# Kernel optimization log

Measured on AMD Instinct MI355X. Metric: run time of the kernel, lower is better.

## Reference

```python
import jax, jax.numpy as jnp
import numpy as np

N = 100000   # nodes
E = 1600000  # edges
D = 64       # in_channels
H = 64       # hidden_channels
G = 1000     # number of graphs (100 nodes each)


def _xavier(key, fan_in, fan_out):
    a = np.sqrt(6.0 / (fan_in + fan_out)).astype(np.float32)
    return jax.random.uniform(key, (fan_in, fan_out), jnp.float32, -a, a)


def setup_inputs() -> dict:
    key = jax.random.key(0)
    ks = jax.random.split(key, 6)
    x = jax.random.normal(ks[0], (N, D), jnp.float32)
    edge_index = jax.random.randint(ks[1], (2, E), 0, N, dtype=jnp.int32)
    edge_weight = jax.random.uniform(ks[2], (E,), jnp.float32)
    # every graph id 0..G-1 occurs exactly N//G times (sorted)
    batch = (jnp.arange(N, dtype=jnp.int32) // (N // G)).astype(jnp.int32)
    W1 = _xavier(ks[3], D, H); b1 = jnp.zeros((H,), jnp.float32)
    W2 = _xavier(ks[4], H, H); b2 = jnp.zeros((H,), jnp.float32)
    W3 = _xavier(ks[5], H, 1); b3 = jnp.zeros((1,), jnp.float32)
    return dict(x=x, edge_index=edge_index, edge_weight=edge_weight, batch=batch,
                W1=W1, b1=b1, W2=W2, b2=b2, W3=W3, b3=b3)


def reference(x, edge_index, edge_weight, batch, W1, b1, W2, b2, W3, b3):
    src, dst = edge_index[0], edge_index[1]
    # nodes per graph (torch.bincount(batch)) and broadcast back to nodes
    counts = jax.ops.segment_sum(jnp.ones((N,), jnp.float32), batch, num_segments=G)
    cpn = counts[batch]  # [N]

    def mpnn_layer(h, W, b):
        # gather x_j, scale by edge weight, scatter-add to target nodes
        m = h[src] * edge_weight[:, None]              # [E, C]
        agg = jax.ops.segment_sum(m, dst, num_segments=N)  # [N, C]
        out = agg / cpn[:, None]                       # per-node normalize
        return out @ W + b

    h = jax.nn.sigmoid(mpnn_layer(x, W1, b1))
    h = jax.nn.sigmoid(mpnn_layer(h, W2, b2))
    h = mpnn_layer(h, W3, b3)                          # [N, 1]
    # global mean pool over each graph
    pooled = jax.ops.segment_sum(h, batch, num_segments=G) / counts[:, None]
    return pooled  # [G, 1]
```

## Files before the change

kernel.cpp:

```cpp
#include <hip/hip_runtime.h>
#include <hip/hip_fp16.h>
#include <math.h>

#define NN 100000
#define EE 1600000
#define GG 1000
#define NPG 100
#define NBUK 391
#define BCAP 4608
#define EPB 8192
#define NBINBLK ((EE + EPB - 1) / EPB)
#define GEMM1BLK ((NN + 127) / 128)
#define GEMM2BLK ((NN + 63) / 64)

typedef __attribute__((ext_vector_type(8))) short short8v;
typedef __attribute__((ext_vector_type(4))) float float4v;

__device__ __forceinline__ unsigned char f32_to_fp8(float a) {
    return (unsigned char)(__builtin_amdgcn_cvt_pk_fp8_f32(a, a, 0, false) & 0xFF);
}
__device__ __forceinline__ float fp8_to_f32(unsigned b) {
    return __builtin_amdgcn_cvt_f32_fp8((int)b, 0);
}
__device__ __forceinline__ unsigned short f32_to_bf16(float f) {
    unsigned u = __float_as_uint(f);
    unsigned r = u + 0x7FFFu + ((u >> 16) & 1u);
    return (unsigned short)(r >> 16);
}

#if __has_builtin(__builtin_amdgcn_cvt_pk_f32_fp8)
typedef float floatx2 __attribute__((ext_vector_type(2)));
#define HAVE_PK_CVT 1
#else
#define HAVE_PK_CVT 0
#endif

__device__ __forceinline__ void unpack4(unsigned dw, float* f) {
#if HAVE_PK_CVT
    floatx2 lo = __builtin_amdgcn_cvt_pk_f32_fp8(dw, false);
    floatx2 hi = __builtin_amdgcn_cvt_pk_f32_fp8(dw, true);
    f[0] = lo.x; f[1] = lo.y; f[2] = hi.x; f[3] = hi.y;
#else
    f[0] = fp8_to_f32(dw & 0xFF);
    f[1] = fp8_to_f32((dw >> 8) & 0xFF);
    f[2] = fp8_to_f32((dw >> 16) & 0xFF);
    f[3] = fp8_to_f32((dw >> 24) & 0xFF);
#endif
}

__device__ __forceinline__ float4v mfma16(short8v a, short8v b, float4v c) {
    return __builtin_amdgcn_mfma_f32_16x16x32_bf16(a, b, c, 0, 0, 0);
}
__device__ __forceinline__ short8v fp8x8_to_bf16frag(uint2 q) {
    float f[8];
    unpack4(q.x, f);
    unpack4(q.y, f + 4);
    short8v s;
#pragma unroll
    for (int j = 0; j < 8; j++) s[j] = (short)f32_to_bf16(f[j]);
    return s;
}
__device__ __forceinline__ short8v f32x8_to_bf16frag(float4 a, float4 b) {
    short8v s;
    s[0] = (short)f32_to_bf16(a.x); s[1] = (short)f32_to_bf16(a.y);
    s[2] = (short)f32_to_bf16(a.z); s[3] = (short)f32_to_bf16(a.w);
    s[4] = (short)f32_to_bf16(b.x); s[5] = (short)f32_to_bf16(b.y);
    s[6] = (short)f32_to_bf16(b.z); s[7] = (short)f32_to_bf16(b.w);
    return s;
}
template<int NT>
__device__ __forceinline__ void stageW(const float* __restrict__ W,
                                       unsigned short* Wt, int tid) {
    for (int i = tid; i < 4096; i += NT) {
        int k = i >> 6, c = i & 63;
        Wt[(c << 6) | (((k >> 3) ^ (c & 7)) << 3) | (k & 7)] = f32_to_bf16(W[i]);
    }
}
__device__ __forceinline__ short8v ldB(const unsigned short* Wt, int col, int g) {
    return *(const short8v*)&Wt[(col << 6) | ((g ^ (col & 7)) << 3)];
}
__device__ __forceinline__ void mfma_tile_store(short8v a_lo, short8v a_hi,
                                                const unsigned short* Wt,
                                                int row0, int lane,
                                                unsigned char* __restrict__ out, int n) {
    int rl = lane & 15, kg = lane >> 4;
#pragma unroll
    for (int ct = 0; ct < 4; ct++) {
        int col = ct * 16 + rl;
        short8v blo = ldB(Wt, col, kg);
        short8v bhi = ldB(Wt, col, 4 + kg);
        float4v acc = {0.f, 0.f, 0.f, 0.f};
        acc = mfma16(a_lo, blo, acc);
        acc = mfma16(a_hi, bhi, acc);
        int dr = (lane >> 4) * 4;
#pragma unroll
        for (int r = 0; r < 4; r++) {
            int R = row0 + dr + r;
            if (R < n) out[(size_t)R * 64 + col] = f32_to_fp8(acc[r]);
        }
    }
}

__global__ __launch_bounds__(512)
void k_binbound(const int* __restrict__ src, const int* __restrict__ dst,
                const float* __restrict__ ew, int* __restrict__ bukcnt,
                uint2* __restrict__ ep1, int* __restrict__ rowptr, int E) {
    __shared__ int hist[NBUK];
    __shared__ int gbase[NBUK];
    int tid = threadIdx.x;
    if (blockIdx.x == 0 && tid == 0) rowptr[NN] = EE;
    for (int i = tid; i < NBUK; i += 512) hist[i] = 0;
    __syncthreads();
    int base = blockIdx.x * EPB;
    int b[16], rank[16];
    unsigned x[16], w[16];
#pragma unroll
    for (int u = 0; u < 16; u++) {
        int e = base + u * 512 + tid;
        if (e < E) {
            int d = dst[e];
            b[u] = d >> 8;
            x[u] = ((unsigned)(d & 255) << 24) | (unsigned)src[e];
            w[u] = __float_as_uint(ew[e]);
            rank[u] = atomicAdd(&hist[b[u]], 1);
        } else b[u] = -1;
    }
    __syncthreads();
    for (int i = tid; i < NBUK; i += 512) {
        int h = hist[i];
        gbase[i] = h ? atomicAdd(&bukcnt[i], h) : 0;
    }
    __syncthreads();
#pragma unroll
    for (int u = 0; u < 16; u++) {
        if (b[u] >= 0) ep1[(size_t)b[u] * BCAP + gbase[b[u]] + rank[u]] = make_uint2(x[u], w[u]);
    }
}

__global__ __launch_bounds__(512)
void k_bin2gemm1(const uint2* __restrict__ ep1, const int* __restrict__ bukcnt,
                 unsigned* __restrict__ ep2, int* __restrict__ rowptr,
                 const float* __restrict__ x, const float* __restrict__ W1,
                 unsigned char* __restrict__ t, int n) {
    __shared__ __align__(16) unsigned char smem[41984];
    int tid = threadIdx.x;
    int bk = blockIdx.x;
    if (bk < NBUK) {
        uint2* stage = (uint2*)smem;
        int* h   = (int*)(smem + 36864);
        int* s   = h + 256;
        int* cur = s + 256;
        int* sc  = cur + 256;
        int v = (tid < NBUK) ? bukcnt[tid] : 0;
        sc[tid] = v;
        __syncthreads();
        for (int off = 1; off < 512; off <<= 1) {
            int tv = (tid >= off) ? sc[tid - off] : 0;
            __syncthreads();
            sc[tid] += tv;
            __syncthreads();
        }
        int cnt = bukcnt[bk];
        int base = sc[bk] - cnt;
        if (tid < 256) h[tid] = 0;
        __syncthreads();
        size_t ebase = (size_t)bk * BCAP;
        for (int e = tid; e < cnt; e += 512) {
            uint2 r = ep1[ebase + e];
            stage[e] = r;
            atomicAdd(&h[r.x >> 24], 1);
        }
        __syncthreads();
        if (tid < 256) s[tid] = h[tid];
        __syncthreads();
        for (int off = 1; off < 256; off <<= 1) {
            int tv = 0;
            if (tid < 256 && tid >= off) tv = s[tid - off];
            __syncthreads();
            if (tid < 256) s[tid] += tv;
            __syncthreads();
        }
        if (tid < 256) {
            int pfx = base + s[tid] - h[tid];
            int node = bk * 256 + tid;
            if (node < n) rowptr[node] = pfx;
            cur[tid] = pfx;
        }
        __syncthreads();
        for (int e = tid; e < cnt; e += 512) {
            uint2 r = stage[e];
            int pos = atomicAdd(&cur[r.x >> 24], 1);
            unsigned wq = (unsigned)fminf(__uint_as_float(r.y) * 32768.f + 0.5f, 32767.f);
            ep2[pos] = (wq << 17) | (r.x & 0x1FFFFu);
        }
    } else {
        unsigned short* Wt = (unsigned short*)smem;
        stageW<512>(W1, Wt, tid);
        __syncthreads();
        int w = tid >> 6, lane = tid & 63;
        int row0 = (bk - NBUK) * 128 + w * 16;
        int rl = lane & 15, kg = lane >> 4;
        int rsrc = row0 + rl;
        if (rsrc > n - 1) rsrc = n - 1;
        const float* ar = x + (size_t)rsrc * 64 + kg * 8;
        float4 f0 = *(const float4*)ar;
        float4 f1 = *(const float4*)(ar + 4);
        float4 f2 = *(const float4*)(ar + 32);
        float4 f3 = *(const float4*)(ar + 36);
        short8v a_lo = f32x8_to_bf16frag(f0, f1);
        short8v a_hi = f32x8_to_bf16frag(f2, f3);
        mfma_tile_store(a_lo, a_hi, Wt, row0, lane, t, n);
    }
}

__global__ __launch_bounds__(256)
void k_gemm64_mfma(const unsigned char* __restrict__ inp, const float* __restrict__ W,
                   unsigned char* __restrict__ out, int n) {
    __shared__ __align__(16) unsigned short Wt[64 * 64];
    int tid = threadIdx.x;
    stageW<256>(W, Wt, tid);
    __syncthreads();
    int w = tid >> 6, lane = tid & 63;
    int row0 = blockIdx.x * 64 + w * 16;
    int rl = lane & 15, kg = lane >> 4;
    int rsrc = row0 + rl;
    if (rsrc > n - 1) rsrc = n - 1;
    const unsigned char* ar = inp + (size_t)rsrc * 64 + kg * 8;
    uint2 qlo = *(const uint2*)ar;
    uint2 qhi = *(const uint2*)(ar + 32);
    short8v a_lo = fp8x8_to_bf16frag(qlo);
    short8v a_hi = fp8x8_to_bf16frag(qhi);
    mfma_tile_store(a_lo, a_hi, Wt, row0, lane, out, n);
}

template<int MODE>
__global__ void k_gather64(const unsigned char* __restrict__ t, const int* __restrict__ rowptr,
                           const unsigned* __restrict__ ep, void* __restrict__ outp,
                           const float* __restrict__ bv, const float* __restrict__ W3,
                           int n) {
    int wid = (blockIdx.x * blockDim.x + threadIdx.x) >> 6;
    int lane = threadIdx.x & 63;
    wid = __builtin_amdgcn_readfirstlane(wid);
    if (wid >= n) return;
    int beg = rowptr[wid], end = rowptr[wid + 1];
    int deg = end - beg;
    float acc0 = 0.f, acc1 = 0.f;
    if (deg > 0) {
        int nfull = deg >> 4;
        int e = beg;
        unsigned r0[16], r1[16];
#pragma unroll
        for (int u = 0; u < 16; u++) r0[u] = ep[e + u];
        for (int b = 0; b < nfull; b++) {
#pragma unroll
            for (int u = 0; u < 16; u++) r1[u] = ep[e + 16 + u];
#pragma unroll
            for (int u = 0; u < 16; u++) {
                unsigned off = (r0[u] & 0x1FFFFu) * 64u + (unsigned)lane;
                float v = fp8_to_f32(t[off]);
                if (u & 1) acc1 = fmaf((float)(r0[u] >> 17), v, acc1);
                else       acc0 = fmaf((float)(r0[u] >> 17), v, acc0);
            }
#pragma unroll
            for (int u = 0; u < 16; u++) r0[u] = r1[u];
            e += 16;
        }
        int rem = deg & 15;
        if (rem) {
#pragma unroll
            for (int u = 0; u < 16; u++) {
                unsigned rm = (u < rem) ? r0[u] : 0u;
                unsigned off = (rm & 0x1FFFFu) * 64u + (unsigned)lane;
                float v = fp8_to_f32(t[off]);
                if (u & 1) acc1 = fmaf((float)(rm >> 17), v, acc1);
                else       acc0 = fmaf((float)(rm >> 17), v, acc0);
            }
        }
    }
    const float C = 0x1p-15f / (float)NPG;
    float v = (acc0 + acc1) * C + bv[lane];
    v = 1.f / (1.f + __expf(-v));
    if (MODE == 0) {
        ((unsigned char*)outp)[(size_t)wid * 64 + lane] = f32_to_fp8(v);
    } else {
        v *= W3[lane];
#pragma unroll
        for (int off = 32; off > 0; off >>= 1) v += __shfl_down(v, off, 64);
        if (lane == 0) ((float*)outp)[wid] = v;
    }
}

__global__ __launch_bounds__(256)
void k_y3pool(const float* __restrict__ y, const int* __restrict__ rowptr,
              const unsigned* __restrict__ ep,
              const float* __restrict__ b3, float* __restrict__ out) {
    __shared__ float red[256];
    int g = blockIdx.x;
    int tid = threadIdx.x;
    int ebeg = rowptr[g * NPG], eend = rowptr[g * NPG + NPG];
    float acc = 0.f;
    for (int e = ebeg + tid; e < eend; e += 256) {
        unsigned r = ep[e];
        unsigned off = (r & 0x1FFFFu) * 4u;
        acc = fmaf((float)(r >> 17), *(const float*)((const char*)y + off), acc);
    }
    red[tid] = acc;
    __syncthreads();
    for (int off = 128; off > 0; off >>= 1) {
        if (tid < off) red[tid] += red[tid + off];
        __syncthreads();
    }
    if (tid == 0) {
        out[g] = red[0] * 0x1p-15f / ((float)NPG * (float)NPG) + b3[0];
    }
}

extern "C" void kernel_launch(void* const* d_in, const int* in_sizes, int n_in,
                              void* d_out, int out_size, void* d_ws, size_t ws_size,
                              hipStream_t stream) {
    const float* x     = (const float*)d_in[0];
    const int*   ei    = (const int*)d_in[1];
    const int*   src   = ei;
    const int*   dst   = ei + EE;
    const float* ew    = (const float*)d_in[2];
    const float* W1    = (const float*)d_in[4];
    const float* b1    = (const float*)d_in[5];
    const float* W2    = (const float*)d_in[6];
    const float* b2    = (const float*)d_in[7];
    const float* W3    = (const float*)d_in[8];
    const float* b3    = (const float*)d_in[9];
    float* out = (float*)d_out;

    unsigned char* t   = (unsigned char*)d_ws;
    unsigned char* t2  = t + (size_t)NN * 64;
    unsigned char* hh8 = t2 + (size_t)NN * 64;
    float* y      = (float*)(hh8 + (size_t)NN * 64);
    unsigned* ep2 = (unsigned*)(y + NN);
    int*   bukcnt = (int*)(ep2 + EE);
    int*   rowptr = bukcnt + NBUK + 1;
    uint2* ep1    = (uint2*)(rowptr + NN + 2);

    hipMemsetAsync(bukcnt, 0, NBUK * sizeof(int), stream);

    k_binbound<<<NBINBLK, 512, 0, stream>>>(src, dst, ew, bukcnt, ep1, rowptr, EE);

    k_bin2gemm1<<<NBUK + GEMM1BLK, 512, 0, stream>>>(ep1, bukcnt, ep2, rowptr, x, W1, t, NN);

    int gblk = (int)(((size_t)NN * 64 + 255) / 256);

    k_gather64<0><<<gblk, 256, 0, stream>>>(t, rowptr, ep2, hh8, b1, nullptr, NN);

    k_gemm64_mfma<<<GEMM2BLK, 256, 0, stream>>>(hh8, W2, t2, NN);

    k_gather64<1><<<gblk, 256, 0, stream>>>(t2, rowptr, ep2, y, b2, W3, NN);

    k_y3pool<<<GG, 256, 0, stream>>>(y, rowptr, ep2, b3, out);
}
```

Baseline: 215.6 us.

## Process 16 nodes per wave in gather with software-pipelined edge chunks

The gather kernel now assigns 16 consecutive destination nodes to each wavefront and streams their CSR edges as one continuous run. Edge words and fp8 feature bytes are double-buffered: the next chunk's loads are issued before the current chunk's FMAs, and each node's epilogue fires when its edge boundary is crossed. This targets per-node launch and tail overhead (waves with few edges, remainder handling) and aims to hide gather latency, at the cost of more registers and a serial boundary check inside the inner loop. Occupancy is also pinned through launch bounds.

```diff
diff --git a/kernel.cpp b/kernel.cpp
--- a/kernel.cpp
+++ b/kernel.cpp
@@ -6,6 +6,7 @@
 #define EE 1600000
 #define GG 1000
 #define NPG 100
+#define NPW 16
 #define NBUK 391
 #define BCAP 4608
 #define EPB 8192
@@ -234,60 +235,92 @@
 }
 
 template<int MODE>
-__global__ void k_gather64(const unsigned char* __restrict__ t, const int* __restrict__ rowptr,
-                           const unsigned* __restrict__ ep, void* __restrict__ outp,
-                           const float* __restrict__ bv, const float* __restrict__ W3,
-                           int n) {
-    int wid = (blockIdx.x * blockDim.x + threadIdx.x) >> 6;
+__global__ __launch_bounds__(256, 4)
+void k_gather64(const unsigned char* __restrict__ t, const int* __restrict__ rowptr,
+                const unsigned* __restrict__ ep, void* __restrict__ outp,
+                const float* __restrict__ bv, const float* __restrict__ W3,
+                int nw) {
+    int gwid = (blockIdx.x * blockDim.x + threadIdx.x) >> 6;
     int lane = threadIdx.x & 63;
-    wid = __builtin_amdgcn_readfirstlane(wid);
-    if (wid >= n) return;
-    int beg = rowptr[wid], end = rowptr[wid + 1];
-    int deg = end - beg;
-    float acc0 = 0.f, acc1 = 0.f;
-    if (deg > 0) {
-        int nfull = deg >> 4;
-        int e = beg;
-        unsigned r0[16], r1[16];
-#pragma unroll
-        for (int u = 0; u < 16; u++) r0[u] = ep[e + u];
-        for (int b = 0; b < nfull; b++) {
-#pragma unroll
-            for (int u = 0; u < 16; u++) r1[u] = ep[e + 16 + u];
-#pragma unroll
-            for (int u = 0; u < 16; u++) {
-                unsigned off = (r0[u] & 0x1FFFFu) * 64u + (unsigned)lane;
-                float v = fp8_to_f32(t[off]);
-                if (u & 1) acc1 = fmaf((float)(r0[u] >> 17), v, acc1);
-                else       acc0 = fmaf((float)(r0[u] >> 17), v, acc0);
-            }
-#pragma unroll
-            for (int u = 0; u < 16; u++) r0[u] = r1[u];
-            e += 16;
-        }
-        int rem = deg & 15;
-        if (rem) {
-#pragma unroll
-            for (int u = 0; u < 16; u++) {
-                unsigned rm = (u < rem) ? r0[u] : 0u;
-                unsigned off = (rm & 0x1FFFFu) * 64u + (unsigned)lane;
-                float v = fp8_to_f32(t[off]);
-                if (u & 1) acc1 = fmaf((float)(rm >> 17), v, acc1);
-                else       acc0 = fmaf((float)(rm >> 17), v, acc0);
-            }
-        }
-    }
-    const float C = 0x1p-15f / (float)NPG;
-    float v = (acc0 + acc1) * C + bv[lane];
-    v = 1.f / (1.f + __expf(-v));
-    if (MODE == 0) {
-        ((unsigned char*)outp)[(size_t)wid * 64 + lane] = f32_to_fp8(v);
-    } else {
-        v *= W3[lane];
-#pragma unroll
-        for (int off = 32; off > 0; off >>= 1) v += __shfl_down(v, off, 64);
-        if (lane == 0) ((float*)outp)[wid] = v;
-    }
+    gwid = __builtin_amdgcn_readfirstlane(gwid);
+    if (gwid >= nw) return;
+    int n0 = gwid * NPW;
+    int n1 = n0 + NPW; if (n1 > NN) n1 = NN;
+    int li = lane < (n1 - n0) ? lane : (n1 - n0);
+    int rv = rowptr[n0 + li];
+    int eb   = __builtin_amdgcn_readfirstlane(__shfl(rv, 0, 64));
+    int eend = __builtin_amdgcn_readfirstlane(__shfl(rv, n1 - n0, 64));
+    int j = n0;
+    int end_j = __builtin_amdgcn_readlane(rv, 1);
+    int nch = (eend - eb + 15) >> 4;
+    float acc = 0.f;
+    const float Cn = 0x1p-15f / (float)NPG;
+    float bvl = bv[lane];
+    float w3l = (MODE == 1) ? W3[lane] : 0.f;
+
+    auto epi = [&]() {
+        float vv = acc * Cn + bvl;
+        vv = 1.f / (1.f + __expf(-vv));
+        if (MODE == 0) {
+            ((unsigned char*)outp)[(size_t)j * 64 + lane] = f32_to_fp8(vv);
+        } else {
+            vv *= w3l;
+            vv += __shfl_down(vv, 32, 64);
+            vv += __shfl_down(vv, 16, 64);
+            vv += __shfl_down(vv, 8, 64);
+            vv += __shfl_down(vv, 4, 64);
+            vv += __shfl_down(vv, 2, 64);
+            vv += __shfl_down(vv, 1, 64);
+            if (lane == 0) ((float*)outp)[j] = vv;
+        }
+        acc = 0.f;
+    };
+
+#define LOADW(W, cc) { _Pragma("unroll") \
+    for (int u = 0; u < 16; u++) W[u] = ep[eb + (cc) * 16 + u]; }
+
+#define ISSUEB(B, WT, W, cc) { _Pragma("unroll") \
+    for (int u = 0; u < 16; u++) { \
+        unsigned wd = (eb + (cc) * 16 + u < eend) ? W[u] : 0u; \
+        WT[u] = (float)(wd >> 17); \
+        B[u] = (unsigned)t[(wd & 0x1FFFFu) * 64u + (unsigned)lane]; \
+    } }
+
+#define FMACHUNK(B, WT, cc) { _Pragma("unroll") \
+    for (int u = 0; u < 16; u++) { \
+        int ee = eb + (cc) * 16 + u; \
+        while (j < n1 && ee == end_j) { \
+            epi(); \
+            j++; \
+            end_j = __builtin_amdgcn_readlane(rv, j - n0 + 1); \
+        } \
+        acc = fmaf(WT[u], fp8_to_f32(B[u]), acc); \
+    } }
+
+    if (nch > 0) {
+        unsigned wA[16], wB[16], b0[16], b1[16];
+        float wt0[16], wt1[16];
+        LOADW(wA, 0);
+        if (nch > 1) LOADW(wB, 1);
+        ISSUEB(b0, wt0, wA, 0);
+        int c = 0;
+        while (true) {
+            if (c + 1 < nch) ISSUEB(b1, wt1, wB, c + 1);
+            if (c + 2 < nch) LOADW(wA, c + 2);
+            FMACHUNK(b0, wt0, c);
+            c++;
+            if (c >= nch) break;
+            if (c + 1 < nch) ISSUEB(b0, wt0, wA, c + 1);
+            if (c + 2 < nch) LOADW(wB, c + 2);
+            FMACHUNK(b1, wt1, c);
+            c++;
+            if (c >= nch) break;
+        }
+    }
+    while (j < n1) { epi(); j++; }
+#undef LOADW
+#undef ISSUEB
+#undef FMACHUNK
 }
 
 __global__ __launch_bounds__(256)
@@ -346,13 +379,14 @@
 
     k_bin2gemm1<<<NBUK + GEMM1BLK, 512, 0, stream>>>(ep1, bukcnt, ep2, rowptr, x, W1, t, NN);
 
-    int gblk = (int)(((size_t)NN * 64 + 255) / 256);
-
-    k_gather64<0><<<gblk, 256, 0, stream>>>(t, rowptr, ep2, hh8, b1, nullptr, NN);
+    int nwv = (NN + NPW - 1) / NPW;
+    int gblk = (nwv * 64 + 255) / 256;
+
+    k_gather64<0><<<gblk, 256, 0, stream>>>(t, rowptr, ep2, hh8, b1, nullptr, nwv);
 
     k_gemm64_mfma<<<GEMM2BLK, 256, 0, stream>>>(hh8, W2, t2, NN);
 
-    k_gather64<1><<<gblk, 256, 0, stream>>>(t2, rowptr, ep2, y, b2, W3, NN);
+    k_gather64<1><<<gblk, 256, 0, stream>>>(t2, rowptr, ep2, y, b2, W3, nwv);
 
     k_y3pool<<<GG, 256, 0, stream>>>(y, rowptr, ep2, b3, out);
 }
```

After: 266.9 us. 1.24x slower.

## Gather 4 fp8 channels per lane across 4 edges with shuffled edge indices

Applied to the files above, without the earlier changes.

Restructures the per-node gather so each wavefront loads up to 64 edge records in one coalesced read and broadcasts them with shuffles. Each lane then reads a 4-byte chunk (4 fp8 channels), so four quarter-waves handle four edges at a time, and the partial sums are combined with xor shuffles. This replaces many byte-wide scalar loads and the per-edge serial loop with wider vector loads and more edges in flight, at the cost of cross-lane reductions and idle lanes for low-degree nodes. The output path packs 4 fp8 values per store, and the final W3 dot product is adjusted to match.

```diff
diff --git a/kernel.cpp b/kernel.cpp
--- a/kernel.cpp
+++ b/kernel.cpp
@@ -234,59 +234,72 @@
 }
 
 template<int MODE>
-__global__ void k_gather64(const unsigned char* __restrict__ t, const int* __restrict__ rowptr,
-                           const unsigned* __restrict__ ep, void* __restrict__ outp,
-                           const float* __restrict__ bv, const float* __restrict__ W3,
-                           int n) {
+__global__ __launch_bounds__(256)
+void k_gather64(const unsigned char* __restrict__ t, const int* __restrict__ rowptr,
+                const unsigned* __restrict__ ep, void* __restrict__ outp,
+                const float* __restrict__ bv, const float* __restrict__ W3,
+                int n) {
     int wid = (blockIdx.x * blockDim.x + threadIdx.x) >> 6;
     int lane = threadIdx.x & 63;
     wid = __builtin_amdgcn_readfirstlane(wid);
     if (wid >= n) return;
     int beg = rowptr[wid], end = rowptr[wid + 1];
-    int deg = end - beg;
-    float acc0 = 0.f, acc1 = 0.f;
-    if (deg > 0) {
-        int nfull = deg >> 4;
-        int e = beg;
-        unsigned r0[16], r1[16];
-#pragma unroll
-        for (int u = 0; u < 16; u++) r0[u] = ep[e + u];
-        for (int b = 0; b < nfull; b++) {
-#pragma unroll
-            for (int u = 0; u < 16; u++) r1[u] = ep[e + 16 + u];
-#pragma unroll
-            for (int u = 0; u < 16; u++) {
-                unsigned off = (r0[u] & 0x1FFFFu) * 64u + (unsigned)lane;
-                float v = fp8_to_f32(t[off]);
-                if (u & 1) acc1 = fmaf((float)(r0[u] >> 17), v, acc1);
-                else       acc0 = fmaf((float)(r0[u] >> 17), v, acc0);
+    int q = lane >> 4;
+    unsigned sl4 = (unsigned)(lane & 15) * 4u;
+    float ax = 0.f, ay = 0.f, az = 0.f, aw = 0.f;
+    for (int base = beg; base < end; base += 64) {
+        int el = base + lane;
+        unsigned wl = 0u;
+        if (el < end) wl = ep[el];
+        int nE = end - base; if (nE > 64) nE = 64;
+        int ng = (nE + 3) >> 2;
+        for (int g0 = 0; g0 < ng; g0 += 4) {
+            unsigned vv[4];
+            float wt[4];
+#pragma unroll
+            for (int p = 0; p < 4; p++) {
+                unsigned wq = __shfl(wl, (g0 + p) * 4 + q, 64);
+                wt[p] = (float)(wq >> 17);
+                vv[p] = *(const unsigned*)(t + ((wq & 0x1FFFFu) * 64u + sl4));
             }
 #pragma unroll
-            for (int u = 0; u < 16; u++) r0[u] = r1[u];
-            e += 16;
-        }
-        int rem = deg & 15;
-        if (rem) {
-#pragma unroll
-            for (int u = 0; u < 16; u++) {
-                unsigned rm = (u < rem) ? r0[u] : 0u;
-                unsigned off = (rm & 0x1FFFFu) * 64u + (unsigned)lane;
-                float v = fp8_to_f32(t[off]);
-                if (u & 1) acc1 = fmaf((float)(rm >> 17), v, acc1);
-                else       acc0 = fmaf((float)(rm >> 17), v, acc0);
+            for (int p = 0; p < 4; p++) {
+                float f[4];
+                unpack4(vv[p], f);
+                ax = fmaf(wt[p], f[0], ax);
+                ay = fmaf(wt[p], f[1], ay);
+                az = fmaf(wt[p], f[2], az);
+                aw = fmaf(wt[p], f[3], aw);
             }
         }
     }
-    const float C = 0x1p-15f / (float)NPG;
-    float v = (acc0 + acc1) * C + bv[lane];
-    v = 1.f / (1.f + __expf(-v));
+    ax += __shfl_xor(ax, 16, 64); ax += __shfl_xor(ax, 32, 64);
+    ay += __shfl_xor(ay, 16, 64); ay += __shfl_xor(ay, 32, 64);
+    az += __shfl_xor(az, 16, 64); az += __shfl_xor(az, 32, 64);
+    aw += __shfl_xor(aw, 16, 64); aw += __shfl_xor(aw, 32, 64);
+
+    const float Cn = 0x1p-15f / (float)NPG;
+    float4 bb = ((const float4*)bv)[lane & 15];
+    float v0 = ax * Cn + bb.x, v1 = ay * Cn + bb.y;
+    float v2 = az * Cn + bb.z, v3 = aw * Cn + bb.w;
+    v0 = 1.f / (1.f + __expf(-v0));
+    v1 = 1.f / (1.f + __expf(-v1));
+    v2 = 1.f / (1.f + __expf(-v2));
+    v3 = 1.f / (1.f + __expf(-v3));
     if (MODE == 0) {
-        ((unsigned char*)outp)[(size_t)wid * 64 + lane] = f32_to_fp8(v);
+        if (q == 0) {
+            unsigned r = (unsigned)__builtin_amdgcn_cvt_pk_fp8_f32(v0, v1, 0, false);
+            r = (unsigned)__builtin_amdgcn_cvt_pk_fp8_f32(v2, v3, (int)r, true);
+            ((unsigned*)outp)[(size_t)wid * 16 + (lane & 15)] = r;
+        }
     } else {
-        v *= W3[lane];
-#pragma unroll
-        for (int off = 32; off > 0; off >>= 1) v += __shfl_down(v, off, 64);
-        if (lane == 0) ((float*)outp)[wid] = v;
+        float4 w4 = ((const float4*)W3)[lane & 15];
+        float d = v0 * w4.x + v1 * w4.y + v2 * w4.z + v3 * w4.w;
+        d += __shfl_xor(d, 1, 64);
+        d += __shfl_xor(d, 2, 64);
+        d += __shfl_xor(d, 4, 64);
+        d += __shfl_xor(d, 8, 64);
+        if (lane == 0) ((float*)outp)[wid] = d;
     }
 }
 
```

New measurement: 214.1 us. No clear change (-0.7%).
